# Kernel optimization log

Measured on AMD Instinct MI355X. Metric: run time of the kernel, lower is better.

## Reference

```python
import jax, jax.numpy as jnp
import numpy as np

DIM_HEADS = 64
NB_FEATURES = 256
KERNEL_EPS = 1e-4


def _gaussian_orthogonal_random_matrix(nb_rows, nb_cols, seed=0):
    # scaling == 1: rows scaled by sqrt(nb_cols); orthogonal QR blocks
    rng = np.random.RandomState(seed)
    nb_full_blocks = nb_rows // nb_cols
    blocks = []
    for _ in range(nb_full_blocks):
        unstructured = rng.randn(nb_cols, nb_cols)
        q, _ = np.linalg.qr(unstructured)
        blocks.append(q.T)
    rem = nb_rows - nb_full_blocks * nb_cols
    if rem > 0:
        unstructured = rng.randn(nb_cols, nb_cols)
        q, _ = np.linalg.qr(unstructured)
        blocks.append(q.T[:rem])
    final = np.concatenate(blocks, axis=0)
    multiplier = np.sqrt(float(nb_cols)) * np.ones((nb_rows,))
    return (multiplier[:, None] * final).astype(np.float32)


def setup_inputs() -> dict:
    key = jax.random.key(0)
    kq, kk, kv = jax.random.split(key, 3)
    b, h, n, d = 4, 16, 4096, DIM_HEADS
    q = jax.random.normal(kq, (b, h, n, d), dtype=jnp.float32)
    k = jax.random.normal(kk, (b, h, n, d), dtype=jnp.float32)
    v = jax.random.normal(kv, (b, h, n, d), dtype=jnp.float32)
    proj = jnp.asarray(_gaussian_orthogonal_random_matrix(NB_FEATURES, d))  # [m, d]
    return {"q": q, "k": k, "v": v, "proj": proj}


def _softmax_kernel(data, proj, is_query, eps=KERNEL_EPS):
    d = data.shape[-1]
    m = proj.shape[0]
    data_normalizer = d ** (-0.25)
    ratio = m ** (-0.5)
    # [b,h,n,m]
    data_dash = jnp.einsum('bhnd,md->bhnm', data_normalizer * data, proj)
    diag_data = jnp.sum(data ** 2, axis=-1, keepdims=True) * 0.5 * data_normalizer ** 2
    if is_query:
        stab = jax.lax.stop_gradient(jnp.max(data_dash, axis=-1, keepdims=True))
    else:
        stab = jax.lax.stop_gradient(jnp.max(data_dash, axis=(-1, -2), keepdims=True))
    return ratio * (jnp.exp(data_dash - diag_data - stab) + eps)


def _linear_attention(q, k, v):
    # q,k: [b,h,n,m] features; v: [b,h,n,e]
    k_cumsum = jnp.sum(k, axis=-2)                               # [b,h,m]
    D_inv = 1.0 / jnp.einsum('bhnm,bhm->bhn', q, k_cumsum)       # [b,h,n]
    context = jnp.einsum('bhnm,bhne->bhme', k, v)                # [b,h,m,e]
    return jnp.einsum('bhme,bhnm,bhn->bhne', context, q, D_inv)  # [b,h,n,e]


def reference(q, k, v, proj):
    q_prime = _softmax_kernel(q, proj, is_query=True)
    k_prime = _softmax_kernel(k, proj, is_query=False)
    return _linear_attention(q_prime, k_prime, v)
```

## Files before the change

### kernel.cpp

```cpp
#include <hip/hip_runtime.h>

#define SEQ 4096
#define CDN 0.35355339059327379f
#define DIAGC 0.0625f
#define KEPS 1e-4f

typedef _Float16 f16;
typedef f16 f16x8 __attribute__((ext_vector_type(8)));
typedef f16 f16x4 __attribute__((ext_vector_type(4)));
typedef float f32x4 __attribute__((ext_vector_type(4)));

#define MFMA16(a, b, c) __builtin_amdgcn_mfma_f32_16x16x32_f16(a, b, c, 0, 0, 0)

#define PSTR 72

__device__ __forceinline__ void stage_proj(const float* __restrict__ proj, f16* plds) {
  int t = threadIdx.x;
  int mrow = t >> 2;
  int cb = (t & 3) * 16;
#pragma unroll
  for (int p = 0; p < 4; ++p) {
    int m = mrow + p * 64;
    const float4* src = (const float4*)(proj + m * 64 + cb);
    f16* dst = plds + m * PSTR + cb;
#pragma unroll
    for (int i = 0; i < 4; ++i) {
      float4 v = src[i];
      f16x4 h = {(f16)v.x, (f16)v.y, (f16)v.z, (f16)v.w};
      *(f16x4*)(dst + i * 4) = h;
    }
  }
}

__device__ __forceinline__ f16x8 proj_frag(const f16* plds, int mtile, int ks, int lane) {
  int m = (lane & 15) + 16 * mtile;
  return *(const f16x8*)(plds + m * PSTR + ks * 32 + (lane >> 4) * 8);
}

__device__ __forceinline__ f16x8 pfrag32(const float* __restrict__ proj, int mt, int ks, int lane) {
  const float4* p = (const float4*)(proj + (size_t)(16 * mt + (lane & 15)) * 64 + ks * 32 + (lane >> 4) * 8);
  float4 a = p[0], b = p[1];
  f16x8 r = {(f16)a.x, (f16)a.y, (f16)a.z, (f16)a.w,
             (f16)b.x, (f16)b.y, (f16)b.z, (f16)b.w};
  return r;
}

__device__ __forceinline__ f16x8 row_frag(const float* __restrict__ base, int lane, int ks, float& sq) {
  const float4* p = (const float4*)(base + (size_t)(lane & 15) * 64 + ks * 32 + (lane >> 4) * 8);
  float4 a = p[0], b = p[1];
  sq += a.x*a.x + a.y*a.y + a.z*a.z + a.w*a.w + b.x*b.x + b.y*b.y + b.z*b.z + b.w*b.w;
  f16x8 r = {(f16)(a.x*CDN), (f16)(a.y*CDN), (f16)(a.z*CDN), (f16)(a.w*CDN),
             (f16)(b.x*CDN), (f16)(b.y*CDN), (f16)(b.z*CDN), (f16)(b.w*CDN)};
  return r;
}

#define VSTR 72

__device__ __forceinline__ void stage_vT(const float* __restrict__ vbh, int n, int e8, int nl, f16* dst) {
  const float4* vp = (const float4*)(vbh + (size_t)n * 64 + e8);
  float4 a = vp[0], b = vp[1];
  dst[(e8 + 0) * VSTR + nl] = (f16)a.x;
  dst[(e8 + 1) * VSTR + nl] = (f16)a.y;
  dst[(e8 + 2) * VSTR + nl] = (f16)a.z;
  dst[(e8 + 3) * VSTR + nl] = (f16)a.w;
  dst[(e8 + 4) * VSTR + nl] = (f16)b.x;
  dst[(e8 + 5) * VSTR + nl] = (f16)b.y;
  dst[(e8 + 6) * VSTR + nl] = (f16)b.z;
  dst[(e8 + 7) * VSTR + nl] = (f16)b.w;
}

__global__ __launch_bounds__(512, 4) void k2_ctx(
    const float* __restrict__ kk, const float* __restrict__ vv,
    const float* __restrict__ proj,
    float* __restrict__ ctx_part, float* __restrict__ kcum_part,
    float* __restrict__ stabm, float* __restrict__ vs_part) {
  __shared__ __align__(16) f16 vt[2][64 * VSTR];
  __shared__ __align__(16) f16 pht[8][16 * 40];
  __shared__ __align__(16) float diag_s[8][32];
  __shared__ float red2[4][16];
  __shared__ float stabs[8];
  int bh = blockIdx.x & 63, rest = blockIdx.x >> 6;
  int mc = rest & 3, ns = rest >> 2;
  int w = threadIdx.x >> 6, lane = threadIdx.x & 63;
  int q4 = lane >> 4, l15 = lane & 15;
  int mtl = w & 3, nsub = w >> 2;
  f16x8 pa0 = pfrag32(proj, mc * 4 + mtl, 0, lane);
  f16x8 pa1 = pfrag32(proj, mc * 4 + mtl, 1, lane);
  const float* kbh = kk + (size_t)bh * SEQ * 64;
  const float* vbh = vv + (size_t)bh * SEQ * 64;
  f32x4 actx[4];
  f32x4 akc = {0.f, 0.f, 0.f, 0.f};
#pragma unroll
  for (int i = 0; i < 4; ++i) actx[i] = (f32x4){0.f, 0.f, 0.f, 0.f};
  float vsacc[4] = {0.f, 0.f, 0.f, 0.f};
  float M = -1e30f;
  f16x8 ones = {(f16)1.f, (f16)1.f, (f16)1.f, (f16)1.f,
                (f16)1.f, (f16)1.f, (f16)1.f, (f16)1.f};
  int nl = threadIdx.x & 63, e8 = (threadIdx.x >> 6) * 8;
  int nbase = ns * 1024;
  stage_vT(vbh, nbase + nl, e8, nl, &vt[0][0]);
  __syncthreads();
#pragma unroll 1
  for (int it = 0; it < 16; ++it) {
    int n0 = nbase + it * 64;
    if (it < 15) stage_vT(vbh, n0 + 64 + nl, e8, nl, &vt[(it & 1) ^ 1][0]);
    const f16* vcur = &vt[it & 1][0];
    f16x8 ak[2][2];
    float dg[2];
#pragma unroll
    for (int nt = 0; nt < 2; ++nt) {
      float sq = 0.f;
      const float* kb = kbh + (size_t)(n0 + nsub * 32 + nt * 16) * 64;
      ak[nt][0] = row_frag(kb, lane, 0, sq);
      ak[nt][1] = row_frag(kb, lane, 1, sq);
      sq += __shfl_xor(sq, 16, 64);
      sq += __shfl_xor(sq, 32, 64);
      dg[nt] = sq * DIAGC;
    }
    if (lane < 16) { diag_s[w][lane] = dg[0]; diag_s[w][16 + lane] = dg[1]; }
    f32x4 accv[2];
#pragma unroll
    for (int nt = 0; nt < 2; ++nt) {
      f32x4 a = {0.f, 0.f, 0.f, 0.f};
      a = MFMA16(ak[nt][0], pa0, a);
      a = MFMA16(ak[nt][1], pa1, a);
      accv[nt] = a;
    }
    float tm = fmaxf(fmaxf(fmaxf(accv[0][0], accv[0][1]), fmaxf(accv[0][2], accv[0][3])),
                     fmaxf(fmaxf(accv[1][0], accv[1][1]), fmaxf(accv[1][2], accv[1][3])));
#pragma unroll
    for (int m = 1; m < 64; m <<= 1) tm = fmaxf(tm, __shfl_xor(tm, m, 64));
    if (tm > M) {
      float rs = __expf(M - tm);
      akc *= rs;
#pragma unroll
      for (int et = 0; et < 4; ++et) actx[et] *= rs;
      M = tm;
    }
#pragma unroll
    for (int nt = 0; nt < 2; ++nt) {
      float4 dgv = ((const float4*)&diag_s[w][0])[nt * 4 + q4];
      f16x4 ph;
      ph[0] = (f16)__expf(accv[nt][0] - dgv.x - M);
      ph[1] = (f16)__expf(accv[nt][1] - dgv.y - M);
      ph[2] = (f16)__expf(accv[nt][2] - dgv.z - M);
      ph[3] = (f16)__expf(accv[nt][3] - dgv.w - M);
      *(f16x4*)(&pht[w][l15 * 40 + nt * 16 + q4 * 4]) = ph;
    }
    f16x8 bv[4];
#pragma unroll
    for (int et = 0; et < 4; ++et)
      bv[et] = *(const f16x8*)(vcur + (l15 + 16 * et) * VSTR + nsub * 32 + q4 * 8);
    if (mc == 0 && mtl == 0) {
#pragma unroll
      for (int et = 0; et < 4; ++et) {
        float s = 0.f;
#pragma unroll
        for (int j = 0; j < 8; ++j) s += (float)bv[et][j];
        vsacc[et] += s;
      }
    }
    f16x8 aph = *(const f16x8*)(&pht[w][l15 * 40 + q4 * 8]);
    akc = MFMA16(aph, ones, akc);
#pragma unroll
    for (int et = 0; et < 4; ++et) actx[et] = MFMA16(aph, bv[et], actx[et]);
    __syncthreads();
  }
  if (lane == 0) stabs[w] = M;
  __syncthreads();
  float Mp = stabs[w ^ 4];
  float Mt = fmaxf(M, Mp);
  {
    float sc = __expf(M - Mt);
    akc *= sc;
#pragma unroll
    for (int et = 0; et < 4; ++et) actx[et] *= sc;
  }
  if (mc == 0 && mtl == 0) {
#pragma unroll
    for (int et = 0; et < 4; ++et) {
      float s = vsacc[et];
      s += __shfl_xor(s, 16, 64);
      s += __shfl_xor(s, 32, 64);
      if (lane < 16)
        vs_part[(size_t)bh * 512 + (ns * 2 + nsub) * 64 + lane + 16 * et] = s;
    }
  }
  float* red = (float*)&vt[0][0];
  if (nsub == 1) {
#pragma unroll
    for (int et = 0; et < 4; ++et)
#pragma unroll
      for (int r = 0; r < 4; ++r)
        red[mtl * 1024 + (q4 * 4 + r) * 64 + l15 + 16 * et] = actx[et][r];
    if (l15 == 0) {
#pragma unroll
      for (int r = 0; r < 4; ++r) red2[mtl][q4 * 4 + r] = akc[r];
    }
  }
  __syncthreads();
  if (nsub == 0) {
    float* cp = ctx_part + (((size_t)bh * 4 + ns) * 256 + mc * 64 + mtl * 16) * 64;
#pragma unroll
    for (int et = 0; et < 4; ++et)
#pragma unroll
      for (int r = 0; r < 4; ++r)
        cp[(size_t)(q4 * 4 + r) * 64 + l15 + 16 * et] =
            actx[et][r] + red[mtl * 1024 + (q4 * 4 + r) * 64 + l15 + 16 * et];
    if (l15 == 0) {
#pragma unroll
      for (int r = 0; r < 4; ++r)
        kcum_part[((size_t)bh * 4 + ns) * 256 + mc * 64 + mtl * 16 + q4 * 4 + r] =
            akc[r] + red2[mtl][q4 * 4 + r];
    }
    if (lane == 0) stabm[(size_t)bh * 64 + ns * 16 + mc * 4 + mtl] = Mt;
  }
}

__global__ __launch_bounds__(256) void k2c_red(
    const float* __restrict__ ctx_part, const float* __restrict__ kcum_part,
    const float* __restrict__ stabm, const float* __restrict__ vs_part,
    float* __restrict__ ws_kcum, f16* __restrict__ ws_ctxT) {
  __shared__ float tile[64 * 65];
  __shared__ float sred[64];
  __shared__ float vsum_l[64];
  __shared__ float fac[4][4];
  int bh = blockIdx.x & 63, mq = blockIdx.x >> 6;
  int t = threadIdx.x;
  if (t < 64) {
    sred[t] = stabm[(size_t)bh * 64 + t];
    float vs = 0.f;
#pragma unroll
    for (int i = 0; i < 8; ++i) vs += vs_part[(size_t)bh * 512 + i * 64 + t];
    vsum_l[t] = vs;
  }
  __syncthreads();
  float S = -1e30f;
#pragma unroll
  for (int i = 0; i < 64; ++i) S = fmaxf(S, sred[i]);
  if (t < 16) fac[t >> 2][t & 3] = __expf(sred[(t >> 2) * 16 + mq * 4 + (t & 3)] - S);
  __syncthreads();
  const float* cp = ctx_part + ((size_t)bh * 4 * 256 + mq * 64) * 64;
#pragma unroll
  for (int i = 0; i < 16; ++i) {
    int idx = t + i * 256;
    int ml = idx >> 6, e = idx & 63;
    int tl = ml >> 4;
    float acc = KEPS * vsum_l[e];
#pragma unroll
    for (int ns = 0; ns < 4; ++ns)
      acc += fac[ns][tl] * cp[(size_t)ns * 16384 + idx];
    tile[ml * 65 + e] = acc;
  }
  if (t < 64) {
    int tl = t >> 4;
    float acc = KEPS * 4096.f;
#pragma unroll
    for (int ns = 0; ns < 4; ++ns)
      acc += fac[ns][tl] * kcum_part[((size_t)bh * 4 + ns) * 256 + mq * 64 + t];
    ws_kcum[bh * 256 + mq * 64 + t] = acc;
  }
  __syncthreads();
  f16* ct = ws_ctxT + (size_t)bh * 16384 + mq * 64;
  int mj = t & 63, eg = t >> 6;
#pragma unroll
  for (int i = 0; i < 16; ++i) {
    int e = eg + i * 4;
    ct[(size_t)e * 256 + mj] = (f16)tile[mj * 65 + e];
  }
}

#define CSTR 264

__global__ __launch_bounds__(256, 2) void k3_out(
    const float* __restrict__ qq, const float* __restrict__ proj,
    const float* __restrict__ ws_kcum, const f16* __restrict__ ws_ctxT,
    float* __restrict__ out) {
  __shared__ __align__(16) f16 plds[256 * PSTR];
  __shared__ __align__(16) f16 ctx_l[64 * CSTR];
  __shared__ __align__(16) f16 phq[4][16 * 72];
  __shared__ __align__(16) float kcl[256];
  int bh = blockIdx.x >> 4, blk = blockIdx.x & 15;
  int t = threadIdx.x;
  stage_proj(proj, plds);
  kcl[t] = ws_kcum[bh * 256 + t];
  {
    const f16* cb = ws_ctxT + (size_t)bh * 16384;
#pragma unroll
    for (int i = 0; i < 8; ++i) {
      int c = t + i * 256;
      int e = c >> 5, mo = (c & 31) * 8;
      *(f16x8*)(ctx_l + e * CSTR + mo) = *(const f16x8*)(cb + e * 256 + mo);
    }
  }
  int w = t >> 6, lane = t & 63;
  int q4 = lane >> 4, l15 = lane & 15;
  const float* qbh = qq + (size_t)bh * SEQ * 64;
  float* obh = out + (size_t)bh * SEQ * 64;
  __syncthreads();
#pragma unroll 1
  for (int it = 0; it < 4; ++it) {
    int n0 = blk * 256 + w * 64 + it * 16;
    float sq = 0.f;
    f16x8 bq0 = row_frag(qbh + (size_t)n0 * 64, lane, 0, sq);
    f16x8 bq1 = row_frag(qbh + (size_t)n0 * 64, lane, 1, sq);
    sq += __shfl_xor(sq, 16, 64);
    sq += __shfl_xor(sq, 32, 64);
    float diag = sq * DIAGC;
    f32x4 dd[16];
#pragma unroll
    for (int mt = 0; mt < 16; ++mt) {
      f32x4 acc = {0.f, 0.f, 0.f, 0.f};
      acc = MFMA16(proj_frag(plds, mt, 0, lane), bq0, acc);
      acc = MFMA16(proj_frag(plds, mt, 1, lane), bq1, acc);
      dd[mt] = acc;
    }
    float st = -1e30f;
#pragma unroll
    for (int mt = 0; mt < 16; ++mt)
      st = fmaxf(st, fmaxf(fmaxf(dd[mt][0], dd[mt][1]), fmaxf(dd[mt][2], dd[mt][3])));
    st = fmaxf(st, __shfl_xor(st, 16, 64));
    st = fmaxf(st, __shfl_xor(st, 32, 64));
    float dacc = 0.f;
    f32x4 ao[4];
#pragma unroll
    for (int r = 0; r < 4; ++r) ao[r] = (f32x4){0.f, 0.f, 0.f, 0.f};
#pragma unroll
    for (int qtr = 0; qtr < 4; ++qtr) {
#pragma unroll
      for (int m2 = 0; m2 < 4; ++m2) {
        int mt = qtr * 4 + m2;
        float4 kc = ((const float4*)kcl)[mt * 4 + q4];
        float e0 = __expf(dd[mt][0] - diag - st) + KEPS;
        float e1 = __expf(dd[mt][1] - diag - st) + KEPS;
        float e2 = __expf(dd[mt][2] - diag - st) + KEPS;
        float e3 = __expf(dd[mt][3] - diag - st) + KEPS;
        dacc += e0 * kc.x + e1 * kc.y + e2 * kc.z + e3 * kc.w;
        f16x4 ph;
        ph[0] = (f16)e0; ph[1] = (f16)e1; ph[2] = (f16)e2; ph[3] = (f16)e3;
        *(f16x4*)(&phq[w][l15 * 72 + m2 * 16 + q4 * 4]) = ph;
      }
#pragma unroll
      for (int kl = 0; kl < 2; ++kl) {
        int ks2 = qtr * 2 + kl;
        f16x8 bph = *(const f16x8*)(&phq[w][l15 * 72 + kl * 32 + q4 * 8]);
#pragma unroll
        for (int rte = 0; rte < 4; ++rte) {
          f16x8 act = *(const f16x8*)(ctx_l + (l15 + 16 * rte) * CSTR + ks2 * 32 + q4 * 8);
          ao[rte] = MFMA16(act, bph, ao[rte]);
        }
      }
    }
    dacc += __shfl_xor(dacc, 16, 64);
    dacc += __shfl_xor(dacc, 32, 64);
    float dinv = 1.0f / dacc;
#pragma unroll
    for (int rte = 0; rte < 4; ++rte) {
      float4 o;
      o.x = ao[rte][0] * dinv;
      o.y = ao[rte][1] * dinv;
      o.z = ao[rte][2] * dinv;
      o.w = ao[rte][3] * dinv;
      *(float4*)(obh + (size_t)(n0 + l15) * 64 + rte * 16 + q4 * 4) = o;
    }
  }
}

extern "C" void kernel_launch(void* const* d_in, const int* in_sizes, int n_in,
                              void* d_out, int out_size, void* d_ws, size_t ws_size,
                              hipStream_t stream) {
  const float* q = (const float*)d_in[0];
  const float* k = (const float*)d_in[1];
  const float* v = (const float*)d_in[2];
  const float* proj = (const float*)d_in[3];
  float* out = (float*)d_out;
  float* ws = (float*)d_ws;
  float* ws_kcum = ws + 1024;
  f16*   ws_ctxT = (f16*)(ws + 17408);
  float* ctx_part  = out;
  float* kcum_part = out + 4194304;
  float* stabm     = out + 4259840;
  float* vs_part   = out + 4263936;
  k2_ctx<<<1024, 512, 0, stream>>>(k, v, proj, ctx_part, kcum_part, stabm, vs_part);
  k2c_red<<<256, 256, 0, stream>>>(ctx_part, kcum_part, stabm, vs_part, ws_kcum, ws_ctxT);
  k3_out<<<1024, 256, 0, stream>>>(q, proj, ws_kcum, ws_ctxT, out);
}
```

Measured before the change: 455.8 us.

## Stage K tiles through LDS cooperatively and recompute query projections instead of holding them

The context kernel now loads each 64-row K tile once per block into double-buffered LDS together with V. It computes the row diag terms cooperatively and folds the data normalizer into the proj fragments, so the two n-subgroup waves no longer each reload and rescale K from global memory. The output kernel drops the 16-tile register array of query projections and recomputes the MFMAs in the second pass, trading extra MFMA work for lower register pressure. Outputs are written with nontemporal stores.

```diff
diff --git a/kernel.cpp b/kernel.cpp
--- a/kernel.cpp
+++ b/kernel.cpp
@@ -37,11 +37,11 @@
   return *(const f16x8*)(plds + m * PSTR + ks * 32 + (lane >> 4) * 8);
 }
 
-__device__ __forceinline__ f16x8 pfrag32(const float* __restrict__ proj, int mt, int ks, int lane) {
+__device__ __forceinline__ f16x8 pfrag32s(const float* __restrict__ proj, int mt, int ks, int lane) {
   const float4* p = (const float4*)(proj + (size_t)(16 * mt + (lane & 15)) * 64 + ks * 32 + (lane >> 4) * 8);
   float4 a = p[0], b = p[1];
-  f16x8 r = {(f16)a.x, (f16)a.y, (f16)a.z, (f16)a.w,
-             (f16)b.x, (f16)b.y, (f16)b.z, (f16)b.w};
+  f16x8 r = {(f16)(a.x*CDN), (f16)(a.y*CDN), (f16)(a.z*CDN), (f16)(a.w*CDN),
+             (f16)(b.x*CDN), (f16)(b.y*CDN), (f16)(b.z*CDN), (f16)(b.w*CDN)};
   return r;
 }
 
@@ -54,19 +54,35 @@
   return r;
 }
 
-#define VSTR 72
-
-__device__ __forceinline__ void stage_vT(const float* __restrict__ vbh, int n, int e8, int nl, f16* dst) {
-  const float4* vp = (const float4*)(vbh + (size_t)n * 64 + e8);
-  float4 a = vp[0], b = vp[1];
-  dst[(e8 + 0) * VSTR + nl] = (f16)a.x;
-  dst[(e8 + 1) * VSTR + nl] = (f16)a.y;
-  dst[(e8 + 2) * VSTR + nl] = (f16)a.z;
-  dst[(e8 + 3) * VSTR + nl] = (f16)a.w;
-  dst[(e8 + 4) * VSTR + nl] = (f16)b.x;
-  dst[(e8 + 5) * VSTR + nl] = (f16)b.y;
-  dst[(e8 + 6) * VSTR + nl] = (f16)b.z;
-  dst[(e8 + 7) * VSTR + nl] = (f16)b.w;
+#define KSTR 72
+
+__device__ __forceinline__ void stage_kv(const float* __restrict__ kbh,
+                                         const float* __restrict__ vbh,
+                                         int n0, f16* ktb, f16* vtb,
+                                         float* diagb, int t) {
+  int r = t >> 3;
+  int c8 = (t & 7) * 8;
+  const float4* kp = (const float4*)(kbh + (size_t)(n0 + r) * 64 + c8);
+  float4 a = kp[0], b = kp[1];
+  float sq = a.x*a.x + a.y*a.y + a.z*a.z + a.w*a.w + b.x*b.x + b.y*b.y + b.z*b.z + b.w*b.w;
+  f16x8 h = {(f16)a.x, (f16)a.y, (f16)a.z, (f16)a.w,
+             (f16)b.x, (f16)b.y, (f16)b.z, (f16)b.w};
+  *(f16x8*)(ktb + r * KSTR + c8) = h;
+  sq += __shfl_xor(sq, 1, 64);
+  sq += __shfl_xor(sq, 2, 64);
+  sq += __shfl_xor(sq, 4, 64);
+  if ((t & 7) == 0) diagb[r] = sq * DIAGC;
+  int nl = t & 63, e8 = (t >> 6) * 8;
+  const float4* vp = (const float4*)(vbh + (size_t)(n0 + nl) * 64 + e8);
+  float4 va = vp[0], vb = vp[1];
+  vtb[(e8 + 0) * KSTR + nl] = (f16)va.x;
+  vtb[(e8 + 1) * KSTR + nl] = (f16)va.y;
+  vtb[(e8 + 2) * KSTR + nl] = (f16)va.z;
+  vtb[(e8 + 3) * KSTR + nl] = (f16)va.w;
+  vtb[(e8 + 4) * KSTR + nl] = (f16)vb.x;
+  vtb[(e8 + 5) * KSTR + nl] = (f16)vb.y;
+  vtb[(e8 + 6) * KSTR + nl] = (f16)vb.z;
+  vtb[(e8 + 7) * KSTR + nl] = (f16)vb.w;
 }
 
 __global__ __launch_bounds__(512, 4) void k2_ctx(
@@ -74,18 +90,20 @@
     const float* __restrict__ proj,
     float* __restrict__ ctx_part, float* __restrict__ kcum_part,
     float* __restrict__ stabm, float* __restrict__ vs_part) {
-  __shared__ __align__(16) f16 vt[2][64 * VSTR];
+  __shared__ __align__(16) f16 kt[2][64 * KSTR];
+  __shared__ __align__(16) f16 vt[2][64 * KSTR];
   __shared__ __align__(16) f16 pht[8][16 * 40];
-  __shared__ __align__(16) float diag_s[8][32];
+  __shared__ float diag_all[2][64];
   __shared__ float red2[4][16];
   __shared__ float stabs[8];
   int bh = blockIdx.x & 63, rest = blockIdx.x >> 6;
   int mc = rest & 3, ns = rest >> 2;
-  int w = threadIdx.x >> 6, lane = threadIdx.x & 63;
+  int t = threadIdx.x;
+  int w = t >> 6, lane = t & 63;
   int q4 = lane >> 4, l15 = lane & 15;
   int mtl = w & 3, nsub = w >> 2;
-  f16x8 pa0 = pfrag32(proj, mc * 4 + mtl, 0, lane);
-  f16x8 pa1 = pfrag32(proj, mc * 4 + mtl, 1, lane);
+  f16x8 pa0 = pfrag32s(proj, mc * 4 + mtl, 0, lane);
+  f16x8 pa1 = pfrag32s(proj, mc * 4 + mtl, 1, lane);
   const float* kbh = kk + (size_t)bh * SEQ * 64;
   const float* vbh = vv + (size_t)bh * SEQ * 64;
   f32x4 actx[4];
@@ -96,28 +114,23 @@
   float M = -1e30f;
   f16x8 ones = {(f16)1.f, (f16)1.f, (f16)1.f, (f16)1.f,
                 (f16)1.f, (f16)1.f, (f16)1.f, (f16)1.f};
-  int nl = threadIdx.x & 63, e8 = (threadIdx.x >> 6) * 8;
   int nbase = ns * 1024;
-  stage_vT(vbh, nbase + nl, e8, nl, &vt[0][0]);
+  stage_kv(kbh, vbh, nbase, &kt[0][0], &vt[0][0], &diag_all[0][0], t);
   __syncthreads();
 #pragma unroll 1
   for (int it = 0; it < 16; ++it) {
     int n0 = nbase + it * 64;
-    if (it < 15) stage_vT(vbh, n0 + 64 + nl, e8, nl, &vt[(it & 1) ^ 1][0]);
-    const f16* vcur = &vt[it & 1][0];
+    int cur = it & 1;
+    if (it < 15)
+      stage_kv(kbh, vbh, n0 + 64, &kt[cur ^ 1][0], &vt[cur ^ 1][0], &diag_all[cur ^ 1][0], t);
+    const f16* ktc = &kt[cur][0];
+    const f16* vcur = &vt[cur][0];
     f16x8 ak[2][2];
-    float dg[2];
 #pragma unroll
     for (int nt = 0; nt < 2; ++nt) {
-      float sq = 0.f;
-      const float* kb = kbh + (size_t)(n0 + nsub * 32 + nt * 16) * 64;
-      ak[nt][0] = row_frag(kb, lane, 0, sq);
-      ak[nt][1] = row_frag(kb, lane, 1, sq);
-      sq += __shfl_xor(sq, 16, 64);
-      sq += __shfl_xor(sq, 32, 64);
-      dg[nt] = sq * DIAGC;
-    }
-    if (lane < 16) { diag_s[w][lane] = dg[0]; diag_s[w][16 + lane] = dg[1]; }
+      ak[nt][0] = *(const f16x8*)(ktc + (nsub * 32 + nt * 16 + l15) * KSTR + q4 * 8);
+      ak[nt][1] = *(const f16x8*)(ktc + (nsub * 32 + nt * 16 + l15) * KSTR + 32 + q4 * 8);
+    }
     f32x4 accv[2];
 #pragma unroll
     for (int nt = 0; nt < 2; ++nt) {
@@ -139,7 +152,7 @@
     }
 #pragma unroll
     for (int nt = 0; nt < 2; ++nt) {
-      float4 dgv = ((const float4*)&diag_s[w][0])[nt * 4 + q4];
+      float4 dgv = ((const float4*)&diag_all[cur][0])[nsub * 8 + nt * 4 + q4];
       f16x4 ph;
       ph[0] = (f16)__expf(accv[nt][0] - dgv.x - M);
       ph[1] = (f16)__expf(accv[nt][1] - dgv.y - M);
@@ -150,7 +163,7 @@
     f16x8 bv[4];
 #pragma unroll
     for (int et = 0; et < 4; ++et)
-      bv[et] = *(const f16x8*)(vcur + (l15 + 16 * et) * VSTR + nsub * 32 + q4 * 8);
+      bv[et] = *(const f16x8*)(vcur + (l15 + 16 * et) * KSTR + nsub * 32 + q4 * 8);
     if (mc == 0 && mtl == 0) {
 #pragma unroll
       for (int et = 0; et < 4; ++et) {
@@ -186,7 +199,7 @@
         vs_part[(size_t)bh * 512 + (ns * 2 + nsub) * 64 + lane + 16 * et] = s;
     }
   }
-  float* red = (float*)&vt[0][0];
+  float* red = (float*)&kt[0][0];
   if (nsub == 1) {
 #pragma unroll
     for (int et = 0; et < 4; ++et)
@@ -307,18 +320,14 @@
     sq += __shfl_xor(sq, 16, 64);
     sq += __shfl_xor(sq, 32, 64);
     float diag = sq * DIAGC;
-    f32x4 dd[16];
+    float st = -1e30f;
 #pragma unroll
     for (int mt = 0; mt < 16; ++mt) {
       f32x4 acc = {0.f, 0.f, 0.f, 0.f};
       acc = MFMA16(proj_frag(plds, mt, 0, lane), bq0, acc);
       acc = MFMA16(proj_frag(plds, mt, 1, lane), bq1, acc);
-      dd[mt] = acc;
-    }
-    float st = -1e30f;
-#pragma unroll
-    for (int mt = 0; mt < 16; ++mt)
-      st = fmaxf(st, fmaxf(fmaxf(dd[mt][0], dd[mt][1]), fmaxf(dd[mt][2], dd[mt][3])));
+      st = fmaxf(st, fmaxf(fmaxf(acc[0], acc[1]), fmaxf(acc[2], acc[3])));
+    }
     st = fmaxf(st, __shfl_xor(st, 16, 64));
     st = fmaxf(st, __shfl_xor(st, 32, 64));
     float dacc = 0.f;
@@ -330,11 +339,14 @@
 #pragma unroll
       for (int m2 = 0; m2 < 4; ++m2) {
         int mt = qtr * 4 + m2;
+        f32x4 acc = {0.f, 0.f, 0.f, 0.f};
+        acc = MFMA16(proj_frag(plds, mt, 0, lane), bq0, acc);
+        acc = MFMA16(proj_frag(plds, mt, 1, lane), bq1, acc);
         float4 kc = ((const float4*)kcl)[mt * 4 + q4];
-        float e0 = __expf(dd[mt][0] - diag - st) + KEPS;
-        float e1 = __expf(dd[mt][1] - diag - st) + KEPS;
-        float e2 = __expf(dd[mt][2] - diag - st) + KEPS;
-        float e3 = __expf(dd[mt][3] - diag - st) + KEPS;
+        float e0 = __expf(acc[0] - diag - st) + KEPS;
+        float e1 = __expf(acc[1] - diag - st) + KEPS;
+        float e2 = __expf(acc[2] - diag - st) + KEPS;
+        float e3 = __expf(acc[3] - diag - st) + KEPS;
         dacc += e0 * kc.x + e1 * kc.y + e2 * kc.z + e3 * kc.w;
         f16x4 ph;
         ph[0] = (f16)e0; ph[1] = (f16)e1; ph[2] = (f16)e2; ph[3] = (f16)e3;
@@ -356,12 +368,8 @@
     float dinv = 1.0f / dacc;
 #pragma unroll
     for (int rte = 0; rte < 4; ++rte) {
-      float4 o;
-      o.x = ao[rte][0] * dinv;
-      o.y = ao[rte][1] * dinv;
-      o.z = ao[rte][2] * dinv;
-      o.w = ao[rte][3] * dinv;
-      *(float4*)(obh + (size_t)(n0 + l15) * 64 + rte * 16 + q4 * 4) = o;
+      f32x4 o = ao[rte] * dinv;
+      __builtin_nontemporal_store(o, (f32x4*)(obh + (size_t)(n0 + l15) * 64 + rte * 16 + q4 * 4));
     }
   }
 }
```

New measurement: 396.2 us. 1.15x faster.
